# Kernel tuning notes

Hardware: AMD Instinct MI355X
Metric: run time of the kernel (lower is better)

The kernel has to match this reference:

```python
import jax, jax.numpy as jnp
import numpy as np

B, L, C, R = 2, 1024, 64, 32
RV, DQK, H, NSINK = 32, 64, 8, 4


def setup_inputs() -> dict:
    key = jax.random.key(0)
    ks = jax.random.split(key, 10)
    s_in = 1.0 / np.sqrt(C * R)
    s_r = 1.0 / np.sqrt(R)
    s_rv = 1.0 / np.sqrt(RV)
    return {
        "x": jax.random.normal(ks[0], (B, L, C, R), jnp.float32),
        "Wq": jax.random.normal(ks[1], (C * R, H * DQK), jnp.float32) * s_in,
        "bq": jax.random.normal(ks[2], (H * DQK,), jnp.float32) * s_in,
        "Wk": jax.random.normal(ks[3], (C * R, DQK), jnp.float32) * s_in,
        "bk": jax.random.normal(ks[4], (DQK,), jnp.float32) * s_in,
        "Wv": jax.random.normal(ks[5], (C, R, RV), jnp.float32) * s_r,
        "bv": jax.random.normal(ks[6], (C, RV), jnp.float32) * s_r,
        "Wo": jax.random.normal(ks[7], (C, RV, R), jnp.float32) * s_rv,
        "bo": jax.random.normal(ks[8], (C, R), jnp.float32) * s_rv,
        "sink_q": jax.random.normal(ks[9], (H, NSINK, DQK), jnp.float32),
    }


def reference(x, Wq, bq, Wk, bk, Wv, bv, Wo, bo, sink_q):
    b, l, c, r = x.shape
    h, d_qk = H, DQK
    scale = 1.0 / np.sqrt(d_qk)

    x_flat = x.reshape(b, l, c * r)
    q = (x_flat @ Wq + bq).reshape(b, l, h, d_qk)          # (B,L,H,D)
    k = x_flat @ Wk + bk                                    # (B,L,D) shared MQA key

    # fp32 softmax over time, as in the original
    logits = (jnp.einsum('blhd,bsd->bhls', q, k).astype(jnp.float32) * scale)
    attn = jax.nn.softmax(logits, axis=-1).astype(x.dtype)  # (B,H,L,S)

    # per-channel value projection (B,L,C,RV)
    v = jnp.einsum('blcr,cro->blco', x, Wv) + bv

    # AV with extra channel axis, fused with head-mean (same math as
    # einsum('bhls,bscv->bhlcv').mean(1))
    y = jnp.einsum('bhls,bscv->blcv', attn, v) / h          # (B,L,C,RV)

    # sink-query branch: learned queries attend over time, mean over (H, S)
    logits_s = (jnp.einsum('hsd,bld->bhsl', sink_q, k).astype(jnp.float32) * scale)
    attn_s = jax.nn.softmax(logits_s, axis=-1).astype(x.dtype)  # (B,H,S,L)
    y_sink = jnp.einsum('bhsl,blcv->bcv', attn_s, v) / (h * NSINK)
    y = y + y_sink[:, None]                                 # broadcast over L

    # per-channel output projection + residual
    y = jnp.einsum('blcv,cvr->blcr', y, Wo) + bo
    return x + y
```

## Files before the change

kernel.cpp:

```cpp
#include <hip/hip_runtime.h>
#include <hip/hip_bf16.h>
#include <math.h>


typedef __attribute__((ext_vector_type(8))) short short8;
typedef __attribute__((ext_vector_type(4))) short short4v;
typedef __attribute__((ext_vector_type(4))) float float4v;

__device__ __forceinline__ short f2b(float f) {
    __hip_bfloat16 h = __float2bfloat16(f);
    return __builtin_bit_cast(short, h);
}
__device__ __forceinline__ float b2f(short s) {
    unsigned u = ((unsigned)(unsigned short)s) << 16;
    return __builtin_bit_cast(float, u);
}

__global__ __launch_bounds__(256) void convert_w_kernel(
    const float* __restrict__ Wq, const float* __restrict__ Wk,
    short* __restrict__ Wt, float* __restrict__ Psink)
{
    const int n0 = blockIdx.x * 64;
    const int k0 = blockIdx.y * 64;
    const int tid = threadIdx.x;
    if (blockIdx.x == 0 && blockIdx.y == 0) {
        #pragma unroll
        for (int p = 0; p < 8; ++p) Psink[p * 256 + tid] = 0.f;
    }
    __shared__ float ts[64][65];
    for (int i = tid; i < 4096; i += 256) {
        int kk = i >> 6, nn = i & 63;
        int n = n0 + nn, k = k0 + kk;
        float v = (n < 512) ? Wq[(long)k * 512 + n] : Wk[(long)k * 64 + (n - 512)];
        ts[kk][nn] = v;
    }
    __syncthreads();
    for (int i = tid; i < 4096; i += 256) {
        int nn = i >> 6, kk = i & 63;
        Wt[(long)(n0 + nn) * 2048 + k0 + kk] = f2b(ts[kk][nn]);
    }
}

__global__ __launch_bounds__(256) void vproj_kernel(
    const float* __restrict__ x, const float* __restrict__ Wv,
    const float* __restrict__ bv, short* __restrict__ vt,
    short* __restrict__ xb)
{
    const int c = blockIdx.x;
    const int chunk = blockIdx.y;
    const int b = chunk >> 4;
    const int l0 = (chunk & 15) * 64;
    const int tid = threadIdx.x;
    __shared__ float Wc[32][33];
    __shared__ float xs[64][33];
    for (int i = tid; i < 1024; i += 256)
        Wc[i >> 5][i & 31] = Wv[(c * 32 + (i >> 5)) * 32 + (i & 31)];
    for (int i = tid; i < 2048; i += 256) {
        int s = i >> 5, r = i & 31;
        long gi = ((long)(b << 10) + l0 + s) * 2048 + c * 32 + r;
        float v = x[gi];
        xs[s][r] = v;
        xb[gi] = f2b(v);
    }
    __syncthreads();
    const int s = tid & 63;
    const int og = tid >> 6;
    #pragma unroll
    for (int oi = 0; oi < 8; ++oi) {
        int o = og * 8 + oi;
        float acc = bv[c * 32 + o];
        #pragma unroll
        for (int r = 0; r < 32; ++r) acc += xs[s][r] * Wc[r][o];
        vt[(long)b * (2048 * 1024) + (long)(c * 32 + o) * 1024 + l0 + s] = f2b(acc);
    }
}

__global__ __launch_bounds__(256) void qkproj_kernel(
    const short* __restrict__ xb, const short* __restrict__ Wt,
    float* __restrict__ qkpart)
{
    __shared__ short As[64][72];
    __shared__ short Bs[64][72];

    const int tid = threadIdx.x;
    const int wave = tid >> 6;
    const int lane = tid & 63;
    const int wm = wave >> 1, wn = wave & 1;
    const int m15 = lane & 15;
    const int quad = lane >> 4;
    const int row0 = blockIdx.y * 64;
    const int col0 = blockIdx.x * 64;
    const int kbase = blockIdx.z * 512;
    float* outz = qkpart + (long)blockIdx.z * 1179648;

    float4v acc[2][2];
    #pragma unroll
    for (int i = 0; i < 2; ++i)
        #pragma unroll
        for (int j = 0; j < 2; ++j)
            #pragma unroll
            for (int r = 0; r < 4; ++r) acc[i][j][r] = 0.f;

    for (int kt = 0; kt < 8; ++kt) {
        int k0 = kbase + kt * 64;
        #pragma unroll
        for (int p = 0; p < 2; ++p) {
            int i = tid + p * 256;
            int m = i >> 3, kq = i & 7;
            *reinterpret_cast<short8*>(&As[m][kq * 8]) =
                *reinterpret_cast<const short8*>(&xb[(long)(row0 + m) * 2048 + k0 + kq * 8]);
        }
        #pragma unroll
        for (int p = 0; p < 2; ++p) {
            int i = tid + p * 256;
            int n = i >> 3, kq = i & 7;
            *reinterpret_cast<short8*>(&Bs[n][kq * 8]) =
                *reinterpret_cast<const short8*>(&Wt[(long)(col0 + n) * 2048 + k0 + kq * 8]);
        }
        __syncthreads();
        #pragma unroll
        for (int ks = 0; ks < 2; ++ks) {
            short8 a[2], b[2];
            #pragma unroll
            for (int t = 0; t < 2; ++t) {
                a[t] = *reinterpret_cast<const short8*>(&As[wm * 32 + t * 16 + m15][ks * 32 + quad * 8]);
                b[t] = *reinterpret_cast<const short8*>(&Bs[wn * 32 + t * 16 + m15][ks * 32 + quad * 8]);
            }
            #pragma unroll
            for (int ti = 0; ti < 2; ++ti)
                #pragma unroll
                for (int tj = 0; tj < 2; ++tj)
                    acc[ti][tj] = __builtin_amdgcn_mfma_f32_16x16x32_bf16(
                        a[ti], b[tj], acc[ti][tj], 0, 0, 0);
        }
        __syncthreads();
    }

    #pragma unroll
    for (int ti = 0; ti < 2; ++ti)
        #pragma unroll
        for (int r = 0; r < 4; ++r) {
            int row = row0 + wm * 32 + ti * 16 + quad * 4 + r;
            #pragma unroll
            for (int tj = 0; tj < 2; ++tj) {
                int col = col0 + wn * 32 + tj * 16 + m15;
                outz[(long)row * 576 + col] = acc[ti][tj][r];
            }
        }
}

__global__ __launch_bounds__(256) void convert_qk_kernel(
    const float* __restrict__ qkpart, const float* __restrict__ bq,
    const float* __restrict__ bk, short* __restrict__ qkb)
{
    int id = blockIdx.x * 256 + threadIdx.x;
    float4 a0 = reinterpret_cast<const float4*>(qkpart)[id];
    float4 a1 = reinterpret_cast<const float4*>(qkpart + 1179648)[id];
    float4 a2 = reinterpret_cast<const float4*>(qkpart + 2359296)[id];
    float4 a3 = reinterpret_cast<const float4*>(qkpart + 3538944)[id];
    int col4 = (id % 144) * 4;
    float4 bias = (col4 < 512)
        ? *reinterpret_cast<const float4*>(&bq[col4])
        : *reinterpret_cast<const float4*>(&bk[col4 - 512]);
    short4v o;
    o[0] = f2b(a0.x + a1.x + a2.x + a3.x + bias.x);
    o[1] = f2b(a0.y + a1.y + a2.y + a3.y + bias.y);
    o[2] = f2b(a0.z + a1.z + a2.z + a3.z + bias.z);
    o[3] = f2b(a0.w + a1.w + a2.w + a3.w + bias.w);
    reinterpret_cast<short4v*>(qkb)[id] = o;
}

__global__ __launch_bounds__(256) void qk_s_kernel(
    const short* __restrict__ qkb, short* __restrict__ S)
{
    const int s0 = blockIdx.x * 64;
    const int l0 = blockIdx.y * 64;
    const int b = blockIdx.z;
    const int tid = threadIdx.x;
    short* Sz = S + ((long)b << 23);

    __shared__ short Qs[64][520];
    __shared__ short Ks[64][72];

    #pragma unroll
    for (int p = 0; p < 16; ++p) {
        int i = tid + p * 256;
        int row = i >> 6, d8 = i & 63;
        *reinterpret_cast<short8*>(&Qs[row][d8 * 8]) =
            *reinterpret_cast<const short8*>(&qkb[(long)((b << 10) + l0 + row) * 576 + d8 * 8]);
    }
    #pragma unroll
    for (int p = 0; p < 2; ++p) {
        int i = tid + p * 256;
        int row = i >> 3, d8 = i & 7;
        *reinterpret_cast<short8*>(&Ks[row][d8 * 8]) =
            *reinterpret_cast<const short8*>(&qkb[(long)((b << 10) + s0 + row) * 576 + 512 + d8 * 8]);
    }
    __syncthreads();

    const int wave = tid >> 6;
    const int lane = tid & 63;
    const int wm = wave >> 1, wn = wave & 1;
    const int m15 = lane & 15;
    const int quad = lane >> 4;

    for (int h = 0; h < 8; ++h) {
        float4v acc[2][2];
        #pragma unroll
        for (int i = 0; i < 2; ++i)
            #pragma unroll
            for (int j = 0; j < 2; ++j)
                #pragma unroll
                for (int r = 0; r < 4; ++r) acc[i][j][r] = 0.f;

        #pragma unroll
        for (int ks = 0; ks < 2; ++ks) {
            short8 a[2], bfr[2];
            #pragma unroll
            for (int t = 0; t < 2; ++t) {
                a[t]   = *reinterpret_cast<const short8*>(
                    &Qs[wm * 32 + t * 16 + m15][h * 64 + ks * 32 + quad * 8]);
                bfr[t] = *reinterpret_cast<const short8*>(
                    &Ks[wn * 32 + t * 16 + m15][ks * 32 + quad * 8]);
            }
            #pragma unroll
            for (int ti = 0; ti < 2; ++ti)
                #pragma unroll
                for (int tj = 0; tj < 2; ++tj)
                    acc[ti][tj] = __builtin_amdgcn_mfma_f32_16x16x32_bf16(
                        a[ti], bfr[tj], acc[ti][tj], 0, 0, 0);
        }

        #pragma unroll
        for (int ti = 0; ti < 2; ++ti)
            #pragma unroll
            for (int r = 0; r < 4; ++r) {
                int l = l0 + wm * 32 + ti * 16 + quad * 4 + r;
                #pragma unroll
                for (int tj = 0; tj < 2; ++tj) {
                    int s = s0 + wn * 32 + tj * 16 + m15;
                    Sz[((long)h << 20) + (l << 10) + s] = f2b(acc[ti][tj][r] * 0.125f);
                }
            }
    }
}

__global__ __launch_bounds__(256) void softmax_avg_kernel(
    const short* __restrict__ S, short* __restrict__ P)
{
    const int l = blockIdx.x;
    const int b = blockIdx.y;
    const int tid = threadIdx.x;
    const int h = tid >> 5, j = tid & 31;
    const short* Sz = S + ((long)b << 23);

    __shared__ float es[8][1032];
    __shared__ float invd[8];

    const short* row = &Sz[((long)h << 20) + (l << 10)];
    float vals[32];
    float pm = -1e30f;
    #pragma unroll
    for (int i = 0; i < 32; ++i) {
        float f = b2f(row[i * 32 + j]);
        vals[i] = f;
        pm = fmaxf(pm, f);
    }
    #pragma unroll
    for (int off = 16; off > 0; off >>= 1) pm = fmaxf(pm, __shfl_down(pm, off, 32));
    pm = __shfl(pm, 0, 32);

    float ps = 0.f;
    #pragma unroll
    for (int i = 0; i < 32; ++i) {
        float e = __expf(vals[i] - pm);
        vals[i] = e;
        ps += e;
    }
    #pragma unroll
    for (int off = 16; off > 0; off >>= 1) ps += __shfl_down(ps, off, 32);
    if (j == 0) invd[h] = 1.f / (8.f * ps);
    __syncthreads();

    const float w = invd[h];
    #pragma unroll
    for (int i = 0; i < 32; ++i) es[h][i * 32 + j] = vals[i] * w;
    __syncthreads();

    for (int s = tid; s < 1024; s += 256) {
        float p = 0.f;
        #pragma unroll
        for (int hh = 0; hh < 8; ++hh) p += es[hh][s];
        P[((long)b << 20) + (l << 10) + s] = f2b(p);
    }
}

__global__ __launch_bounds__(256) void sink_kernel(
    const float* __restrict__ sink_q, const short* __restrict__ qkb,
    float* __restrict__ Psink)
{
    const int z = blockIdx.x;
    const int b = z >> 5;
    const int idx = z & 31;
    const int tid = threadIdx.x;

    __shared__ float sq[64];
    __shared__ float lgl[1024];
    __shared__ float red[4];
    __shared__ float mxs, invs;

    if (tid < 64) sq[tid] = sink_q[idx * 64 + tid];
    __syncthreads();

    float lmax = -1e30f;
    for (int l = tid; l < 1024; l += 256) {
        const short* kp = &qkb[(long)((b << 10) + l) * 576 + 512];
        float acc = 0.f;
        #pragma unroll
        for (int d8 = 0; d8 < 8; ++d8) {
            short8 kv = *reinterpret_cast<const short8*>(&kp[d8 * 8]);
            #pragma unroll
            for (int j = 0; j < 8; ++j) acc += b2f(kv[j]) * sq[d8 * 8 + j];
        }
        acc *= 0.125f;
        lgl[l] = acc;
        lmax = fmaxf(lmax, acc);
    }
    #pragma unroll
    for (int off = 32; off > 0; off >>= 1) lmax = fmaxf(lmax, __shfl_down(lmax, off, 64));
    if ((tid & 63) == 0) red[tid >> 6] = lmax;
    __syncthreads();
    if (tid == 0) mxs = fmaxf(fmaxf(red[0], red[1]), fmaxf(red[2], red[3]));
    __syncthreads();

    const float m = mxs;
    float psum = 0.f;
    for (int l = tid; l < 1024; l += 256) {
        float e = __expf(lgl[l] - m);
        lgl[l] = e;
        psum += e;
    }
    #pragma unroll
    for (int off = 32; off > 0; off >>= 1) psum += __shfl_down(psum, off, 64);
    if ((tid & 63) == 0) red[tid >> 6] = psum;
    __syncthreads();
    if (tid == 0) invs = 1.f / (red[0] + red[1] + red[2] + red[3]);
    __syncthreads();

    const float wgt = invs * (1.f / 32.f);
    for (int l = tid; l < 1024; l += 256)
        atomicAdd(&Psink[(b << 10) + l], lgl[l] * wgt);
}

__global__ __launch_bounds__(256) void sinky_kernel(
    const float* __restrict__ Psink, const short* __restrict__ vt,
    float* __restrict__ Ysink)
{
    const int b = blockIdx.y;
    const int tid = threadIdx.x;
    __shared__ float ps[1024];
    {
        float4 v = reinterpret_cast<const float4*>(&Psink[b << 10])[tid];
        *reinterpret_cast<float4*>(&ps[tid * 4]) = v;
    }
    __syncthreads();
    const int wave = tid >> 6;
    const int lane = tid & 63;
    const int co = blockIdx.x * 4 + wave;
    const short* vp = &vt[((long)b * 2048 + co) * 1024];
    float acc = 0.f;
    #pragma unroll
    for (int t = 0; t < 16; ++t) {
        int l = t * 64 + lane;
        acc += ps[l] * b2f(vp[l]);
    }
    #pragma unroll
    for (int off = 32; off > 0; off >>= 1) acc += __shfl_down(acc, off, 64);
    if (lane == 0) Ysink[(b << 11) + co] = acc;
}

__global__ __launch_bounds__(256) void y_fused_kernel(
    const short* __restrict__ P, const short* __restrict__ vt,
    const float* __restrict__ Ysink, const float* __restrict__ Wo,
    const float* __restrict__ bo, const float* __restrict__ x,
    float* __restrict__ out)
{
    __shared__ short As[128][72];
    __shared__ short Bs[64][72];

    const int tid = threadIdx.x;
    const int b = blockIdx.z;
    const int col0 = blockIdx.x * 64;
    const int row0 = blockIdx.y * 128;
    const short* Pz = P + ((long)b << 20);
    const short* Vz = vt + ((long)b * 2048 * 1024);

    const int wave = tid >> 6;
    const int lane = tid & 63;
    const int wm = wave >> 1, wn = wave & 1;
    const int m15 = lane & 15;
    const int quad = lane >> 4;

    float4v acc[4][2];
    #pragma unroll
    for (int i = 0; i < 4; ++i)
        #pragma unroll
        for (int j = 0; j < 2; ++j)
            #pragma unroll
            for (int r = 0; r < 4; ++r) acc[i][j][r] = 0.f;

    for (int kt = 0; kt < 16; ++kt) {
        int k0 = kt * 64;
        #pragma unroll
        for (int p = 0; p < 4; ++p) {
            int i = tid + p * 256;
            int m = i >> 3, kq = i & 7;
            *reinterpret_cast<short8*>(&As[m][kq * 8]) =
                *reinterpret_cast<const short8*>(&Pz[(long)(row0 + m) * 1024 + k0 + kq * 8]);
        }
        #pragma unroll
        for (int p = 0; p < 2; ++p) {
            int i = tid + p * 256;
            int n = i >> 3, kq = i & 7;
            *reinterpret_cast<short8*>(&Bs[n][kq * 8]) =
                *reinterpret_cast<const short8*>(&Vz[(long)(col0 + n) * 1024 + k0 + kq * 8]);
        }
        __syncthreads();
        #pragma unroll
        for (int ks = 0; ks < 2; ++ks) {
            short8 a[4], bb[2];
            #pragma unroll
            for (int t = 0; t < 4; ++t)
                a[t] = *reinterpret_cast<const short8*>(&As[wm * 64 + t * 16 + m15][ks * 32 + quad * 8]);
            #pragma unroll
            for (int t = 0; t < 2; ++t)
                bb[t] = *reinterpret_cast<const short8*>(&Bs[wn * 32 + t * 16 + m15][ks * 32 + quad * 8]);
            #pragma unroll
            for (int ti = 0; ti < 4; ++ti)
                #pragma unroll
                for (int tj = 0; tj < 2; ++tj)
                    acc[ti][tj] = __builtin_amdgcn_mfma_f32_16x16x32_bf16(
                        a[ti], bb[tj], acc[ti][tj], 0, 0, 0);
        }
        __syncthreads();
    }

    float ysv[2];
    #pragma unroll
    for (int tj = 0; tj < 2; ++tj)
        ysv[tj] = Ysink[(b << 11) + col0 + wn * 32 + tj * 16 + m15];

    #pragma unroll
    for (int ti = 0; ti < 4; ++ti)
        #pragma unroll
        for (int r = 0; r < 4; ++r) {
            int row = wm * 64 + ti * 16 + quad * 4 + r;
            #pragma unroll
            for (int tj = 0; tj < 2; ++tj) {
                int col = wn * 32 + tj * 16 + m15;
                As[row][col] = f2b(acc[ti][tj][r] + ysv[tj]);
            }
        }
    const int c0 = col0 >> 5;
    for (int i = tid; i < 4096; i += 256) {
        int n = i >> 6, k = i & 63;
        short v = 0;
        if ((n >> 5) == (k >> 5))
            v = f2b(Wo[((long)(c0 + (n >> 5)) * 32 + (k & 31)) * 32 + (n & 31)]);
        Bs[n][k] = v;
    }
    __syncthreads();

    float4v acc2[4][2];
    #pragma unroll
    for (int i = 0; i < 4; ++i)
        #pragma unroll
        for (int j = 0; j < 2; ++j)
            #pragma unroll
            for (int r = 0; r < 4; ++r) acc2[i][j][r] = 0.f;

    #pragma unroll
    for (int ks = 0; ks < 2; ++ks) {
        short8 a[4], bb[2];
        #pragma unroll
        for (int t = 0; t < 4; ++t)
            a[t] = *reinterpret_cast<const short8*>(&As[wm * 64 + t * 16 + m15][ks * 32 + quad * 8]);
        #pragma unroll
        for (int t = 0; t < 2; ++t)
            bb[t] = *reinterpret_cast<const short8*>(&Bs[wn * 32 + t * 16 + m15][ks * 32 + quad * 8]);
        #pragma unroll
        for (int ti = 0; ti < 4; ++ti)
            #pragma unroll
            for (int tj = 0; tj < 2; ++tj)
                acc2[ti][tj] = __builtin_amdgcn_mfma_f32_16x16x32_bf16(
                    a[ti], bb[tj], acc2[ti][tj], 0, 0, 0);
    }

    float bov[2];
    #pragma unroll
    for (int tj = 0; tj < 2; ++tj)
        bov[tj] = bo[col0 + wn * 32 + tj * 16 + m15];

    #pragma unroll
    for (int ti = 0; ti < 4; ++ti)
        #pragma unroll
        for (int r = 0; r < 4; ++r) {
            int row = (b << 10) + row0 + wm * 64 + ti * 16 + quad * 4 + r;
            #pragma unroll
            for (int tj = 0; tj < 2; ++tj) {
                int col = col0 + wn * 32 + tj * 16 + m15;
                long oi = (long)row * 2048 + col;
                out[oi] = x[oi] + bov[tj] + acc2[ti][tj][r];
            }
        }
}

extern "C" void kernel_launch(void* const* d_in, const int* in_sizes, int n_in,
                              void* d_out, int out_size, void* d_ws, size_t ws_size,
                              hipStream_t stream)
{
    const float* x  = (const float*)d_in[0];
    const float* Wq = (const float*)d_in[1];
    const float* bq = (const float*)d_in[2];
    const float* Wk = (const float*)d_in[3];
    const float* bk = (const float*)d_in[4];
    const float* Wv = (const float*)d_in[5];
    const float* bv = (const float*)d_in[6];
    const float* Wo = (const float*)d_in[7];
    const float* bo = (const float*)d_in[8];
    const float* sq = (const float*)d_in[9];
    float* out = (float*)d_out;

    float* ws = (float*)d_ws;
    float* qkpart = ws;
    short* qkb    = (short*)(ws + 4718592);
    short* P      = (short*)(ws + 5308416);
    float* Psink  = ws + 6356992;
    short* vt     = (short*)(ws + 6359040);
    float* Ysink  = ws + 8456192;
    float* region = ws + 8460288;
    short* xb     = (short*)region;
    short* Wt     = (short*)(region + 2097152);
    short* Sb     = (short*)region;

    dim3 blk(256);

    convert_w_kernel<<<dim3(9, 32), blk, 0, stream>>>(Wq, Wk, Wt, Psink);
    vproj_kernel<<<dim3(64, 32), blk, 0, stream>>>(x, Wv, bv, vt, xb);
    qkproj_kernel<<<dim3(9, 32, 4), blk, 0, stream>>>(xb, Wt, qkpart);
    convert_qk_kernel<<<dim3(1152), blk, 0, stream>>>(qkpart, bq, bk, qkb);
    qk_s_kernel<<<dim3(16, 16, 2), blk, 0, stream>>>(qkb, Sb);
    softmax_avg_kernel<<<dim3(1024, 2), blk, 0, stream>>>(Sb, P);
    sink_kernel<<<dim3(64), blk, 0, stream>>>(sq, qkb, Psink);
    sinky_kernel<<<dim3(512, 2), blk, 0, stream>>>(Psink, vt, Ysink);
    y_fused_kernel<<<dim3(32, 8, 2), blk, 0, stream>>>(
        P, vt, Ysink, Wo, bo, x, out);
}
```

Measured before the change: 186.0 us.

## Fuse exponentiation and row-sum into QK kernel, drop max-subtraction in softmax

```diff
diff --git a/kernel.cpp b/kernel.cpp
--- a/kernel.cpp
+++ b/kernel.cpp
@@ -18,14 +18,21 @@
 
 __global__ __launch_bounds__(256) void convert_w_kernel(
     const float* __restrict__ Wq, const float* __restrict__ Wk,
-    short* __restrict__ Wt, float* __restrict__ Psink)
+    short* __restrict__ Wt, float* __restrict__ Psink,
+    float* __restrict__ sums)
 {
     const int n0 = blockIdx.x * 64;
     const int k0 = blockIdx.y * 64;
     const int tid = threadIdx.x;
-    if (blockIdx.x == 0 && blockIdx.y == 0) {
-        #pragma unroll
-        for (int p = 0; p < 8; ++p) Psink[p * 256 + tid] = 0.f;
+    if (blockIdx.y == 0) {
+        if (blockIdx.x == 0) {
+            #pragma unroll
+            for (int p = 0; p < 8; ++p) Psink[p * 256 + tid] = 0.f;
+        } else {
+            int base = (blockIdx.x - 1) * 2048;
+            #pragma unroll
+            for (int p = 0; p < 8; ++p) sums[base + p * 256 + tid] = 0.f;
+        }
     }
     __shared__ float ts[64][65];
     for (int i = tid; i < 4096; i += 256) {
@@ -170,8 +177,9 @@
     reinterpret_cast<short4v*>(qkb)[id] = o;
 }
 
-__global__ __launch_bounds__(256) void qk_s_kernel(
-    const short* __restrict__ qkb, short* __restrict__ S)
+__global__ __launch_bounds__(256) void qk_exp_kernel(
+    const short* __restrict__ qkb, short* __restrict__ S,
+    float* __restrict__ sums)
 {
     const int s0 = blockIdx.x * 64;
     const int l0 = blockIdx.y * 64;
@@ -179,16 +187,11 @@
     const int tid = threadIdx.x;
     short* Sz = S + ((long)b << 23);
 
-    __shared__ short Qs[64][520];
+    __shared__ short Qh[64][72];
     __shared__ short Ks[64][72];
-
-    #pragma unroll
-    for (int p = 0; p < 16; ++p) {
-        int i = tid + p * 256;
-        int row = i >> 6, d8 = i & 63;
-        *reinterpret_cast<short8*>(&Qs[row][d8 * 8]) =
-            *reinterpret_cast<const short8*>(&qkb[(long)((b << 10) + l0 + row) * 576 + d8 * 8]);
-    }
+    __shared__ short Rp[64][72];
+    __shared__ float ssum[8][64];
+
     #pragma unroll
     for (int p = 0; p < 2; ++p) {
         int i = tid + p * 256;
@@ -196,7 +199,11 @@
         *reinterpret_cast<short8*>(&Ks[row][d8 * 8]) =
             *reinterpret_cast<const short8*>(&qkb[(long)((b << 10) + s0 + row) * 576 + 512 + d8 * 8]);
     }
-    __syncthreads();
+    {
+        int h = tid >> 5, c = tid & 31;
+        ssum[h][c] = 0.f;
+        ssum[h][32 + c] = 0.f;
+    }
 
     const int wave = tid >> 6;
     const int lane = tid & 63;
@@ -205,6 +212,15 @@
     const int quad = lane >> 4;
 
     for (int h = 0; h < 8; ++h) {
+        #pragma unroll
+        for (int p = 0; p < 2; ++p) {
+            int i = tid + p * 256;
+            int row = i >> 3, d8 = i & 7;
+            *reinterpret_cast<short8*>(&Qh[row][d8 * 8]) =
+                *reinterpret_cast<const short8*>(&qkb[(long)((b << 10) + l0 + row) * 576 + h * 64 + d8 * 8]);
+        }
+        __syncthreads();
+
         float4v acc[2][2];
         #pragma unroll
         for (int i = 0; i < 2; ++i)
@@ -218,10 +234,8 @@
             short8 a[2], bfr[2];
             #pragma unroll
             for (int t = 0; t < 2; ++t) {
-                a[t]   = *reinterpret_cast<const short8*>(
-                    &Qs[wm * 32 + t * 16 + m15][h * 64 + ks * 32 + quad * 8]);
-                bfr[t] = *reinterpret_cast<const short8*>(
-                    &Ks[wn * 32 + t * 16 + m15][ks * 32 + quad * 8]);
+                a[t]   = *reinterpret_cast<const short8*>(&Qh[wm * 32 + t * 16 + m15][ks * 32 + quad * 8]);
+                bfr[t] = *reinterpret_cast<const short8*>(&Ks[wn * 32 + t * 16 + m15][ks * 32 + quad * 8]);
             }
             #pragma unroll
             for (int ti = 0; ti < 2; ++ti)
@@ -232,67 +246,76 @@
         }
 
         #pragma unroll
-        for (int ti = 0; ti < 2; ++ti)
+        for (int ti = 0; ti < 2; ++ti) {
+            float e0[4], e1[4], rs[4];
             #pragma unroll
             for (int r = 0; r < 4; ++r) {
-                int l = l0 + wm * 32 + ti * 16 + quad * 4 + r;
+                e0[r] = __expf(acc[ti][0][r] * 0.125f);
+                e1[r] = __expf(acc[ti][1][r] * 0.125f);
+                rs[r] = e0[r] + e1[r];
+            }
+            int row = wm * 32 + ti * 16 + quad * 4;
+            #pragma unroll
+            for (int r = 0; r < 4; ++r) {
+                Rp[row + r][wn * 32 + m15]      = f2b(e0[r]);
+                Rp[row + r][wn * 32 + 16 + m15] = f2b(e1[r]);
+            }
+            #pragma unroll
+            for (int off = 8; off > 0; off >>= 1)
                 #pragma unroll
-                for (int tj = 0; tj < 2; ++tj) {
-                    int s = s0 + wn * 32 + tj * 16 + m15;
-                    Sz[((long)h << 20) + (l << 10) + s] = f2b(acc[ti][tj][r] * 0.125f);
-                }
-            }
-    }
-}
-
-__global__ __launch_bounds__(256) void softmax_avg_kernel(
-    const short* __restrict__ S, short* __restrict__ P)
+                for (int r = 0; r < 4; ++r)
+                    rs[r] += __shfl_down(rs[r], off, 16);
+            if (m15 == 0) {
+                #pragma unroll
+                for (int r = 0; r < 4; ++r)
+                    atomicAdd(&ssum[h][row + r], rs[r]);
+            }
+        }
+        __syncthreads();
+        #pragma unroll
+        for (int p = 0; p < 2; ++p) {
+            int i = tid + p * 256;
+            int row = i >> 3, c8 = i & 7;
+            *reinterpret_cast<short8*>(&Sz[((long)h << 20) + ((long)(l0 + row) << 10) + s0 + c8 * 8]) =
+                *reinterpret_cast<const short8*>(&Rp[row][c8 * 8]);
+        }
+    }
+    __syncthreads();
+    {
+        int h = tid >> 5, c = tid & 31;
+        atomicAdd(&sums[((long)(b * 8 + h) << 10) + l0 + c], ssum[h][c]);
+        atomicAdd(&sums[((long)(b * 8 + h) << 10) + l0 + 32 + c], ssum[h][32 + c]);
+    }
+}
+
+__global__ __launch_bounds__(256) void pavg_kernel(
+    const float* __restrict__ sums, const short* __restrict__ S,
+    short* __restrict__ P)
 {
     const int l = blockIdx.x;
     const int b = blockIdx.y;
     const int tid = threadIdx.x;
-    const int h = tid >> 5, j = tid & 31;
     const short* Sz = S + ((long)b << 23);
 
-    __shared__ float es[8][1032];
-    __shared__ float invd[8];
-
-    const short* row = &Sz[((long)h << 20) + (l << 10)];
-    float vals[32];
-    float pm = -1e30f;
-    #pragma unroll
-    for (int i = 0; i < 32; ++i) {
-        float f = b2f(row[i * 32 + j]);
-        vals[i] = f;
-        pm = fmaxf(pm, f);
-    }
-    #pragma unroll
-    for (int off = 16; off > 0; off >>= 1) pm = fmaxf(pm, __shfl_down(pm, off, 32));
-    pm = __shfl(pm, 0, 32);
-
-    float ps = 0.f;
-    #pragma unroll
-    for (int i = 0; i < 32; ++i) {
-        float e = __expf(vals[i] - pm);
-        vals[i] = e;
-        ps += e;
-    }
-    #pragma unroll
-    for (int off = 16; off > 0; off >>= 1) ps += __shfl_down(ps, off, 32);
-    if (j == 0) invd[h] = 1.f / (8.f * ps);
-    __syncthreads();
-
-    const float w = invd[h];
-    #pragma unroll
-    for (int i = 0; i < 32; ++i) es[h][i * 32 + j] = vals[i] * w;
-    __syncthreads();
-
-    for (int s = tid; s < 1024; s += 256) {
-        float p = 0.f;
-        #pragma unroll
-        for (int hh = 0; hh < 8; ++hh) p += es[hh][s];
-        P[((long)b << 20) + (l << 10) + s] = f2b(p);
-    }
+    __shared__ float w[8];
+    if (tid < 8) w[tid] = 1.f / (8.f * sums[((long)(b * 8 + tid) << 10) + l]);
+    __syncthreads();
+
+    const int s = tid * 4;
+    float p0 = 0.f, p1 = 0.f, p2 = 0.f, p3 = 0.f;
+    #pragma unroll
+    for (int h = 0; h < 8; ++h) {
+        short4v v = *reinterpret_cast<const short4v*>(
+            &Sz[((long)h << 20) + ((long)l << 10) + s]);
+        float wh = w[h];
+        p0 += wh * b2f(v[0]);
+        p1 += wh * b2f(v[1]);
+        p2 += wh * b2f(v[2]);
+        p3 += wh * b2f(v[3]);
+    }
+    short4v o;
+    o[0] = f2b(p0); o[1] = f2b(p1); o[2] = f2b(p2); o[3] = f2b(p3);
+    *reinterpret_cast<short4v*>(&P[((long)b << 20) + ((long)l << 10) + s]) = o;
 }
 
 __global__ __launch_bounds__(256) void sink_kernel(
@@ -538,19 +561,20 @@
     float* Psink  = ws + 6356992;
     short* vt     = (short*)(ws + 6359040);
     float* Ysink  = ws + 8456192;
-    float* region = ws + 8460288;
+    float* sums   = ws + 8460288;
+    float* region = ws + 8476672;
     short* xb     = (short*)region;
     short* Wt     = (short*)(region + 2097152);
     short* Sb     = (short*)region;
 
     dim3 blk(256);
 
-    convert_w_kernel<<<dim3(9, 32), blk, 0, stream>>>(Wq, Wk, Wt, Psink);
+    convert_w_kernel<<<dim3(9, 32), blk, 0, stream>>>(Wq, Wk, Wt, Psink, sums);
     vproj_kernel<<<dim3(64, 32), blk, 0, stream>>>(x, Wv, bv, vt, xb);
     qkproj_kernel<<<dim3(9, 32, 4), blk, 0, stream>>>(xb, Wt, qkpart);
     convert_qk_kernel<<<dim3(1152), blk, 0, stream>>>(qkpart, bq, bk, qkb);
-    qk_s_kernel<<<dim3(16, 16, 2), blk, 0, stream>>>(qkb, Sb);
-    softmax_avg_kernel<<<dim3(1024, 2), blk, 0, stream>>>(Sb, P);
+    qk_exp_kernel<<<dim3(16, 16, 2), blk, 0, stream>>>(qkb, Sb, sums);
+    pavg_kernel<<<dim3(1024, 2), blk, 0, stream>>>(sums, Sb, P);
     sink_kernel<<<dim3(64), blk, 0, stream>>>(sq, qkb, Psink);
     sinky_kernel<<<dim3(512, 2), blk, 0, stream>>>(Psink, vt, Ysink);
     y_fused_kernel<<<dim3(32, 8, 2), blk, 0, stream>>>(
```

Result: slower. 192.0 us (+3.2%).
